# Performance work log

Measured on AMD Instinct MI355X. Metric: run time of the kernel, lower is better.

The kernel has to match this reference:

```python
import jax, jax.numpy as jnp
import numpy as np

KERNEL = 3072
STRIDE = 512


def setup_inputs() -> dict:
    key = jax.random.key(0)
    ks = jax.random.split(key, 8)
    B, Cin, L = 8, 4, 524288
    Cout, H = 512, 512
    return {
        "input": jax.random.normal(ks[0], (B, Cin, L), jnp.float32),
        "hidden": jnp.zeros((1, B, H), jnp.float32),
        "conv_w": jax.random.normal(ks[1], (Cout, Cin, KERNEL), jnp.float32) * 0.01,
        "conv_b": jax.random.normal(ks[2], (Cout,), jnp.float32) * 0.01,
        "w_ih": jax.random.normal(ks[3], (3 * H, Cout), jnp.float32) * 0.04,
        "w_hh": jax.random.normal(ks[4], (3 * H, H), jnp.float32) * 0.04,
        "b_ih": jax.random.normal(ks[5], (3 * H,), jnp.float32) * 0.04,
        "b_hh": jax.random.normal(ks[6], (3 * H,), jnp.float32) * 0.04,
    }


def _gru_scan(x_tbc, h0, w_ih, w_hh, b_ih, b_hh):
    # PyTorch GRU cell semantics, batched over B, scanned over T.
    # Precompute input projections for all timesteps: [T, B, 3H]
    gi = jnp.einsum('tbc,gc->tbg', x_tbc, w_ih) + b_ih

    def step(h, gi_t):
        gh = h @ w_hh.T + b_hh  # [B, 3H]
        i_r, i_z, i_n = jnp.split(gi_t, 3, axis=-1)
        h_r, h_z, h_n = jnp.split(gh, 3, axis=-1)
        r = jax.nn.sigmoid(i_r + h_r)
        z = jax.nn.sigmoid(i_z + h_z)
        n = jnp.tanh(i_n + r * h_n)
        h_new = (1.0 - z) * n + z * h
        return h_new, h_new

    hT, ys = jax.lax.scan(step, h0, gi)
    return ys, hT


def reference(input, hidden, conv_w, conv_b, w_ih, w_hh, b_ih, b_hh):
    # Conv1d stem: [B, Cin, L] -> [B, Cout, T]
    out = jax.lax.conv_general_dilated(
        input, conv_w, window_strides=(STRIDE,), padding='VALID',
        dimension_numbers=('NCH', 'OIH', 'NCH'))
    out = out + conv_b[None, :, None]
    # dropout is identity in eval mode
    x = jnp.moveaxis(out, 2, 0)  # [T, B, Cout]
    h0 = hidden[0]  # [B, H]
    ys, hT = _gru_scan(x, h0, w_ih, w_hh, b_ih, b_hh)  # ys: [T, B, H]
    T, B, H = ys.shape
    # torch.cat of T tensors [1, B, H] along dim=1 -> [1, T*B, H]
    return ys.reshape(1, T * B, H), hT[None]
```

## Files before the change

kernel.cpp:

```cpp
#include <hip/hip_runtime.h>
#include <hip/hip_fp16.h>
#include <hip/hip_bf16.h>

#define TSTEPS 1019
#define BATCH 8
#define CIN 4
#define LEN 524288
#define COUT 512
#define HID 512
#define KERN 3072
#define CSTRIDE 512
#define KTOT (CIN * KERN)
#define MROWS (TSTEPS * BATCH)

typedef _Float16 half2_v __attribute__((ext_vector_type(2)));
typedef __attribute__((ext_vector_type(8))) short bf16x8;
typedef __attribute__((ext_vector_type(4))) float f32x4;

#if defined(__has_builtin)
#if __has_builtin(__builtin_amdgcn_fdot2)
#define HAVE_FDOT2 1
#endif
#endif

__device__ __forceinline__ float dot2f(__half2 a, __half2 b, float c) {
#ifdef HAVE_FDOT2
    return __builtin_amdgcn_fdot2(__builtin_bit_cast(half2_v, a),
                                  __builtin_bit_cast(half2_v, b), c, false);
#else
    float2 af = __half22float2(a), bf = __half22float2(b);
    return fmaf(af.y, bf.y, fmaf(af.x, bf.x, c));
#endif
}

struct __align__(16) H2x4 { __half2 x, y, z, w; };

__device__ __forceinline__ short bfc(float x) {
    return (short)__builtin_bit_cast(unsigned short, __float2bfloat16(x));
}

__device__ __forceinline__ void load_lds16(const unsigned short* g, unsigned short* l) {
    __builtin_amdgcn_global_load_lds(
        (const __attribute__((address_space(1))) void*)g,
        (__attribute__((address_space(3))) void*)l, 16, 0, 0);
}

__global__ __launch_bounds__(256) void f2bf_k(
        const float* __restrict__ a, unsigned short* __restrict__ o, int n4) {
    int i = blockIdx.x * blockDim.x + threadIdx.x;
    int stride = gridDim.x * blockDim.x;
    for (; i < n4; i += stride) {
        float4 f = reinterpret_cast<const float4*>(a)[i];
        ushort4 u;
        u.x = (unsigned short)bfc(f.x); u.y = (unsigned short)bfc(f.y);
        u.z = (unsigned short)bfc(f.z); u.w = (unsigned short)bfc(f.w);
        reinterpret_cast<ushort4*>(o)[i] = u;
    }
}

__global__ __launch_bounds__(256, 2) void conv_mfma_k(
        const float* __restrict__ in, const unsigned short* __restrict__ wb,
        const float* __restrict__ bias, unsigned short* __restrict__ out) {
    __shared__ unsigned short At[2][128 * 64];
    __shared__ unsigned short Bt[2][128 * 64];
    const int m0 = blockIdx.y * 128;
    const int n0 = blockIdx.x * 128;
    const int tid = threadIdx.x;
    const int w = tid >> 6, l = tid & 63;
    const int wm = w >> 1, wn = w & 1;
    const int fr = l & 15, fq = l >> 4;

    const int ra = tid >> 1, hh = tid & 1;
    int mA = m0 + ra; if (mA > MROWS - 1) mA = MROWS - 1;
    const int tA = mA >> 3, bA = mA & 7;

    f32x4 acc[4][4] = {};

    const int NT = KTOT / 64;

    {
        const int k0 = 0, ci = 0, kr = 0;
        const float* src = in + (size_t)(bA * CIN + ci) * LEN
                              + (size_t)tA * CSTRIDE + kr + hh * 32;
        #pragma unroll
        for (int cc = 0; cc < 4; ++cc) {
            float4 f0 = reinterpret_cast<const float4*>(src)[cc * 2];
            float4 f1 = reinterpret_cast<const float4*>(src)[cc * 2 + 1];
            bf16x8 v;
            v[0] = bfc(f0.x); v[1] = bfc(f0.y); v[2] = bfc(f0.z); v[3] = bfc(f0.w);
            v[4] = bfc(f1.x); v[5] = bfc(f1.y); v[6] = bfc(f1.z); v[7] = bfc(f1.w);
            const int c = hh * 4 + cc, s = c ^ (ra & 7);
            *reinterpret_cast<bf16x8*>(&At[0][ra * 64 + s * 8]) = v;
        }
        #pragma unroll
        for (int i = 0; i < 4; ++i) {
            const int rb = w * 32 + i * 8 + (l >> 3);
            const int s = l & 7, c = s ^ (rb & 7);
            load_lds16(wb + (size_t)(n0 + rb) * KTOT + k0 + c * 8,
                       &Bt[0][(w * 32 + i * 8) * 64]);
        }
    }
    __syncthreads();

    int cur = 0;
    for (int t = 0; t < NT; ++t) {
        const int nxt = cur ^ 1;
        float4 fA[8];
        const bool more = (t + 1 < NT);
        if (more) {
            const int k0 = (t + 1) * 64;
            const int ci = k0 / KERN, kr = k0 - ci * KERN;
            const float* src = in + (size_t)(bA * CIN + ci) * LEN
                                  + (size_t)tA * CSTRIDE + kr + hh * 32;
            #pragma unroll
            for (int v = 0; v < 8; ++v)
                fA[v] = reinterpret_cast<const float4*>(src)[v];
            #pragma unroll
            for (int i = 0; i < 4; ++i) {
                const int rb = w * 32 + i * 8 + (l >> 3);
                const int s = l & 7, c = s ^ (rb & 7);
                load_lds16(wb + (size_t)(n0 + rb) * KTOT + k0 + c * 8,
                           &Bt[nxt][(w * 32 + i * 8) * 64]);
            }
        }
        #pragma unroll
        for (int ks = 0; ks < 2; ++ks) {
            bf16x8 af[4], bfg[4];
            #pragma unroll
            for (int mf = 0; mf < 4; ++mf) {
                const int rA = wm * 64 + mf * 16 + fr;
                const int cw = ks * 4 + fq, s = cw ^ (rA & 7);
                af[mf] = *reinterpret_cast<const bf16x8*>(&At[cur][rA * 64 + s * 8]);
            }
            #pragma unroll
            for (int nf = 0; nf < 4; ++nf) {
                const int rB = wn * 64 + nf * 16 + fr;
                const int cw = ks * 4 + fq, s = cw ^ (rB & 7);
                bfg[nf] = *reinterpret_cast<const bf16x8*>(&Bt[cur][rB * 64 + s * 8]);
            }
            #pragma unroll
            for (int mf = 0; mf < 4; ++mf)
                #pragma unroll
                for (int nf = 0; nf < 4; ++nf)
                    acc[mf][nf] = __builtin_amdgcn_mfma_f32_16x16x32_bf16(
                        af[mf], bfg[nf], acc[mf][nf], 0, 0, 0);
        }
        if (more) {
            #pragma unroll
            for (int cc = 0; cc < 4; ++cc) {
                float4 f0 = fA[cc * 2], f1 = fA[cc * 2 + 1];
                bf16x8 v;
                v[0] = bfc(f0.x); v[1] = bfc(f0.y); v[2] = bfc(f0.z); v[3] = bfc(f0.w);
                v[4] = bfc(f1.x); v[5] = bfc(f1.y); v[6] = bfc(f1.z); v[7] = bfc(f1.w);
                const int c = hh * 4 + cc, s = c ^ (ra & 7);
                *reinterpret_cast<bf16x8*>(&At[nxt][ra * 64 + s * 8]) = v;
            }
        }
        __syncthreads();
        cur = nxt;
    }

    #pragma unroll
    for (int nf = 0; nf < 4; ++nf) {
        const int n = n0 + wn * 64 + nf * 16 + fr;
        const float bv = bias[n];
        #pragma unroll
        for (int mf = 0; mf < 4; ++mf) {
            #pragma unroll
            for (int i = 0; i < 4; ++i) {
                const int m = m0 + wm * 64 + mf * 16 + fq * 4 + i;
                if (m < MROWS)
                    out[(size_t)m * COUT + n] =
                        (unsigned short)bfc(acc[mf][nf][i] + bv);
            }
        }
    }
}

__global__ __launch_bounds__(256, 2) void proj_mfma_k(
        const unsigned short* __restrict__ A, const unsigned short* __restrict__ wb,
        const float* __restrict__ bias, float* __restrict__ out) {
    __shared__ unsigned short At[2][128 * 64];
    __shared__ unsigned short Bt[2][128 * 64];
    const int m0 = blockIdx.y * 128;
    const int n0 = blockIdx.x * 128;
    const int tid = threadIdx.x;
    const int w = tid >> 6, l = tid & 63;
    const int wm = w >> 1, wn = w & 1;
    const int fr = l & 15, fq = l >> 4;

    f32x4 acc[4][4] = {};
    const int NT = COUT / 64;

    auto stage = [&](int buf, int k0) {
        #pragma unroll
        for (int i = 0; i < 4; ++i) {
            const int r = w * 32 + i * 8 + (l >> 3);
            const int s = l & 7, c = s ^ (r & 7);
            int mA = m0 + r; if (mA > MROWS - 1) mA = MROWS - 1;
            load_lds16(A + (size_t)mA * COUT + k0 + c * 8,
                       &At[buf][(w * 32 + i * 8) * 64]);
            load_lds16(wb + (size_t)(n0 + r) * COUT + k0 + c * 8,
                       &Bt[buf][(w * 32 + i * 8) * 64]);
        }
    };

    stage(0, 0);
    __syncthreads();
    int cur = 0;
    for (int t = 0; t < NT; ++t) {
        const int nxt = cur ^ 1;
        if (t + 1 < NT) stage(nxt, (t + 1) * 64);
        #pragma unroll
        for (int ks = 0; ks < 2; ++ks) {
            bf16x8 af[4], bfg[4];
            #pragma unroll
            for (int mf = 0; mf < 4; ++mf) {
                const int rA = wm * 64 + mf * 16 + fr;
                const int cw = ks * 4 + fq, s = cw ^ (rA & 7);
                af[mf] = *reinterpret_cast<const bf16x8*>(&At[cur][rA * 64 + s * 8]);
            }
            #pragma unroll
            for (int nf = 0; nf < 4; ++nf) {
                const int rB = wn * 64 + nf * 16 + fr;
                const int cw = ks * 4 + fq, s = cw ^ (rB & 7);
                bfg[nf] = *reinterpret_cast<const bf16x8*>(&Bt[cur][rB * 64 + s * 8]);
            }
            #pragma unroll
            for (int mf = 0; mf < 4; ++mf)
                #pragma unroll
                for (int nf = 0; nf < 4; ++nf)
                    acc[mf][nf] = __builtin_amdgcn_mfma_f32_16x16x32_bf16(
                        af[mf], bfg[nf], acc[mf][nf], 0, 0, 0);
        }
        __syncthreads();
        cur = nxt;
    }

    #pragma unroll
    for (int nf = 0; nf < 4; ++nf) {
        const int n = n0 + wn * 64 + nf * 16 + fr;
        const float bv = bias[n];
        #pragma unroll
        for (int mf = 0; mf < 4; ++mf) {
            #pragma unroll
            for (int i = 0; i < 4; ++i) {
                const int m = m0 + wm * 64 + mf * 16 + fq * 4 + i;
                if (m < MROWS)
                    out[(size_t)m * 1536 + n] = acc[mf][nf][i] + bv;
            }
        }
    }
}

__global__ __launch_bounds__(512, 1) void gru_scan_k(
        const float* __restrict__ gi, const float* __restrict__ w_hh,
        const float* __restrict__ b_hh, const float* __restrict__ hidden,
        float* __restrict__ out, unsigned long long* __restrict__ h_ex) {
    const int bid = blockIdx.x;
    const int b   = bid & 7;
    const int isl = bid >> 3;
    const int tid = threadIdx.x;
    const int q   = tid >> 7;
    const int g   = tid & 127;
    const int j   = isl * 128 + g;

    __shared__ __align__(16) __half2 hh2[256];
    __shared__ float p_lds[1920];

    __half2 wreg[3][64];
    #pragma unroll
    for (int m = 0; m < 3; ++m) {
        const float* wp = w_hh + (size_t)(j + m * 512) * HID + q * 128;
        #pragma unroll
        for (int kk = 0; kk < 32; ++kk) {
            float4 v = reinterpret_cast<const float4*>(wp)[kk];
            wreg[m][2 * kk]     = __halves2half2(__float2half_rn(v.x), __float2half_rn(v.y));
            wreg[m][2 * kk + 1] = __halves2half2(__float2half_rn(v.z), __float2half_rn(v.w));
        }
    }

    float bhr = 0.f, bhz = 0.f, bhn = 0.f, hprev = 0.f;
    if (tid < 128) {
        bhr = b_hh[j]; bhz = b_hh[j + 512]; bhn = b_hh[j + 1024];
        hprev = hidden[b * HID + j];
    }
    if (tid < 256) {
        float h0a = hidden[b * HID + 2 * tid];
        float h0b = hidden[b * HID + 2 * tid + 1];
        hh2[tid] = __halves2half2(__float2half(h0a), __float2half(h0b));
    }
    __syncthreads();

    float gir = 0.f, giz = 0.f, gin = 0.f;
    if (tid < 128) {
        const float* gp = gi + (size_t)b * 1536 + j;
        gir = gp[0]; giz = gp[512]; gin = gp[1024];
    }

    for (int t = 0; t < TSTEPS; ++t) {
        const H2x4* hv4 = reinterpret_cast<const H2x4*>(hh2 + q * 64);
        float a0 = 0, a1 = 0, a2 = 0, c0 = 0, c1 = 0, c2 = 0;
        #pragma unroll
        for (int kk = 0; kk < 16; ++kk) {
            H2x4 h4 = hv4[kk];
            a0 = dot2f(wreg[0][4 * kk + 0], h4.x, a0);
            a1 = dot2f(wreg[1][4 * kk + 0], h4.x, a1);
            a2 = dot2f(wreg[2][4 * kk + 0], h4.x, a2);
            c0 = dot2f(wreg[0][4 * kk + 1], h4.y, c0);
            c1 = dot2f(wreg[1][4 * kk + 1], h4.y, c1);
            c2 = dot2f(wreg[2][4 * kk + 1], h4.y, c2);
            a0 = dot2f(wreg[0][4 * kk + 2], h4.z, a0);
            a1 = dot2f(wreg[1][4 * kk + 2], h4.z, a1);
            a2 = dot2f(wreg[2][4 * kk + 2], h4.z, a2);
            c0 = dot2f(wreg[0][4 * kk + 3], h4.w, c0);
            c1 = dot2f(wreg[1][4 * kk + 3], h4.w, c1);
            c2 = dot2f(wreg[2][4 * kk + 3], h4.w, c2);
        }
        p_lds[(0 * 128 + g) * 5 + q] = a0 + c0;
        p_lds[(1 * 128 + g) * 5 + q] = a1 + c1;
        p_lds[(2 * 128 + g) * 5 + q] = a2 + c2;
        __syncthreads();

        float hnew = 0.f;
        if (tid < 128) {
            const float* pr = &p_lds[(0 * 128 + tid) * 5];
            const float* pz = &p_lds[(1 * 128 + tid) * 5];
            const float* pn = &p_lds[(2 * 128 + tid) * 5];
            const float ghr = pr[0] + pr[1] + pr[2] + pr[3] + bhr;
            const float ghz = pz[0] + pz[1] + pz[2] + pz[3] + bhz;
            const float ghn = pn[0] + pn[1] + pn[2] + pn[3] + bhn;
            const float r = 1.f / (1.f + __expf(-(gir + ghr)));
            const float z = 1.f / (1.f + __expf(-(giz + ghz)));
            const float nx = gin + r * ghn;
            const float n = 1.f - 2.f / (__expf(2.f * nx) + 1.f);
            hnew = (1.f - z) * n + z * hprev;
            hprev = hnew;
            out[(size_t)(t * BATCH + b) * HID + j] = hnew;
            float hother = __shfl_xor(hnew, 1);
            if (!(tid & 1) && t < TSTEPS - 1) {
                unsigned long long* pub = h_ex
                    + (size_t)(((t + 1) & 1) * BATCH + b) * 256
                    + isl * 64 + (tid >> 1);
                __half2 h2 = __halves2half2(__float2half(hnew), __float2half(hother));
                unsigned long long v =
                    ((unsigned long long)(unsigned)(t + 1) << 32) |
                    (unsigned long long)__builtin_bit_cast(unsigned, h2);
                __hip_atomic_store(pub, v, __ATOMIC_RELAXED,
                                   __HIP_MEMORY_SCOPE_AGENT);
            }
        }
        if (t == TSTEPS - 1) break;

        if (tid < 128) {
            const float* gp = gi + (size_t)((t + 1) * BATCH + b) * 1536 + j;
            gir = gp[0]; giz = gp[512]; gin = gp[1024];
        }

        if (tid < 256) {
            unsigned long long* src = h_ex
                + (size_t)(((t + 1) & 1) * BATCH + b) * 256 + tid;
            unsigned long long v;
            do {
                v = __hip_atomic_load(src, __ATOMIC_RELAXED,
                                      __HIP_MEMORY_SCOPE_AGENT);
            } while ((unsigned)(v >> 32) != (unsigned)(t + 1));
            hh2[tid] = __builtin_bit_cast(__half2, (unsigned)(v & 0xffffffffu));
        }
        __syncthreads();
    }
    if (tid < 128)
        out[(size_t)TSTEPS * BATCH * HID + b * HID + j] = hprev;
}

extern "C" void kernel_launch(void* const* d_in, const int* in_sizes, int n_in,
                              void* d_out, int out_size, void* d_ws, size_t ws_size,
                              hipStream_t stream) {
    (void)in_sizes; (void)n_in; (void)out_size; (void)ws_size;
    const float* input  = (const float*)d_in[0];
    const float* hidden = (const float*)d_in[1];
    const float* conv_w = (const float*)d_in[2];
    const float* conv_b = (const float*)d_in[3];
    const float* w_ih   = (const float*)d_in[4];
    const float* w_hh   = (const float*)d_in[5];
    const float* b_ih   = (const float*)d_in[6];
    const float* b_hh   = (const float*)d_in[7];
    float* out = (float*)d_out;

    char* ws = (char*)d_ws;
    float*          gi       = (float*)ws;
    unsigned short* conv_out = (unsigned short*)(ws + 50085888);
    unsigned short* w_bf     = (unsigned short*)(ws + 58433536);
    unsigned short* wih_bf   = (unsigned short*)(ws + 71016448);
    unsigned long long* h_ex = (unsigned long long*)(ws + 72589312);

    f2bf_k<<<2048, 256, 0, stream>>>(conv_w, w_bf, KTOT * COUT / 4);
    f2bf_k<<<768, 256, 0, stream>>>(w_ih, wih_bf, 1536 * COUT / 4);

    dim3 cgrid(4, 64);
    conv_mfma_k<<<cgrid, 256, 0, stream>>>(input, w_bf, conv_b, conv_out);

    dim3 pgrid(12, 64);
    proj_mfma_k<<<pgrid, 256, 0, stream>>>(conv_out, wih_bf, b_ih, gi);

    hipMemsetAsync(h_ex, 0, 32768, stream);

    gru_scan_k<<<32, 512, 0, stream>>>(gi, w_hh, b_hh, hidden, out, h_ex);
}
```

Measured before the change: 2.208 ms.

## Interleave two batch rows per GRU block to overlap polling with compute

The GRU scan is re-partitioned so that each block handles two batch rows and a 64-wide hidden slice instead of one row and a 128-wide slice. Rows are grouped into teams of 8 blocks. Each block alternates between its two rows within a timestep, so waiting for the other blocks' hidden state for one row overlaps with the matvec and gates of the other row. The per-thread register weight slice is halved, and the partial-sum reduction grows from 4 to 8 terms. In exchange there are more barriers per step, and the block count and launch config may need to match the unseen host code.

Result: slower. 3.178 ms (+43.9%).

```diff
diff --git a/kernel.cpp b/kernel.cpp
--- a/kernel.cpp
+++ b/kernel.cpp
@@ -75,13 +75,11 @@
     const int tA = mA >> 3, bA = mA & 7;
 
     f32x4 acc[4][4] = {};
-
     const int NT = KTOT / 64;
 
     {
-        const int k0 = 0, ci = 0, kr = 0;
-        const float* src = in + (size_t)(bA * CIN + ci) * LEN
-                              + (size_t)tA * CSTRIDE + kr + hh * 32;
+        const float* src = in + (size_t)(bA * CIN + 0) * LEN
+                              + (size_t)tA * CSTRIDE + 0 + hh * 32;
         #pragma unroll
         for (int cc = 0; cc < 4; ++cc) {
             float4 f0 = reinterpret_cast<const float4*>(src)[cc * 2];
@@ -96,7 +94,7 @@
         for (int i = 0; i < 4; ++i) {
             const int rb = w * 32 + i * 8 + (l >> 3);
             const int s = l & 7, c = s ^ (rb & 7);
-            load_lds16(wb + (size_t)(n0 + rb) * KTOT + k0 + c * 8,
+            load_lds16(wb + (size_t)(n0 + rb) * KTOT + 0 + c * 8,
                        &Bt[0][(w * 32 + i * 8) * 64]);
         }
     }
@@ -253,124 +251,145 @@
     }
 }
 
+#define MATVEC(PB)                                                            \
+    do {                                                                      \
+        const H2x4* hv4 = reinterpret_cast<const H2x4*>(&hh2[PB][q * 32]);    \
+        float a0 = 0, a1 = 0, a2 = 0, c0 = 0, c1 = 0, c2 = 0;                 \
+        _Pragma("unroll")                                                     \
+        for (int kk = 0; kk < 8; ++kk) {                                      \
+            H2x4 h4 = hv4[kk];                                                \
+            a0 = dot2f(wreg[0][4 * kk + 0], h4.x, a0);                        \
+            a1 = dot2f(wreg[1][4 * kk + 0], h4.x, a1);                        \
+            a2 = dot2f(wreg[2][4 * kk + 0], h4.x, a2);                        \
+            c0 = dot2f(wreg[0][4 * kk + 1], h4.y, c0);                        \
+            c1 = dot2f(wreg[1][4 * kk + 1], h4.y, c1);                        \
+            c2 = dot2f(wreg[2][4 * kk + 1], h4.y, c2);                        \
+            a0 = dot2f(wreg[0][4 * kk + 2], h4.z, a0);                        \
+            a1 = dot2f(wreg[1][4 * kk + 2], h4.z, a1);                        \
+            a2 = dot2f(wreg[2][4 * kk + 2], h4.z, a2);                        \
+            c0 = dot2f(wreg[0][4 * kk + 3], h4.w, c0);                        \
+            c1 = dot2f(wreg[1][4 * kk + 3], h4.w, c1);                        \
+            c2 = dot2f(wreg[2][4 * kk + 3], h4.w, c2);                        \
+        }                                                                     \
+        p_lds[(0 * 64 + g) * 9 + q] = a0 + c0;                                \
+        p_lds[(1 * 64 + g) * 9 + q] = a1 + c1;                                \
+        p_lds[(2 * 64 + g) * 9 + q] = a2 + c2;                                \
+    } while (0)
+
+#define GATE_PHASE(PB, BB)                                                    \
+    do {                                                                      \
+        const float* pr = &p_lds[(0 * 64 + tid) * 9];                         \
+        const float* pz = &p_lds[(1 * 64 + tid) * 9];                         \
+        const float* pn = &p_lds[(2 * 64 + tid) * 9];                         \
+        const float ghr = ((pr[0] + pr[1]) + (pr[2] + pr[3]))                 \
+                        + ((pr[4] + pr[5]) + (pr[6] + pr[7])) + bhr;          \
+        const float ghz = ((pz[0] + pz[1]) + (pz[2] + pz[3]))                 \
+                        + ((pz[4] + pz[5]) + (pz[6] + pz[7])) + bhz;          \
+        const float ghn = ((pn[0] + pn[1]) + (pn[2] + pn[3]))                 \
+                        + ((pn[4] + pn[5]) + (pn[6] + pn[7])) + bhn;          \
+        const float r = 1.f / (1.f + __expf(-(gir##PB + ghr)));               \
+        const float z = 1.f / (1.f + __expf(-(giz##PB + ghz)));               \
+        const float nx = gin##PB + r * ghn;                                   \
+        const float n = 1.f - 2.f / (__expf(2.f * nx) + 1.f);                 \
+        const float hnew = (1.f - z) * n + z * hprev##PB;                     \
+        hprev##PB = hnew;                                                     \
+        const float hother = __shfl_xor(hnew, 1);                             \
+        if (!(tid & 1)) {                                                     \
+            __half2 h2 = __halves2half2(__float2half(hnew),                   \
+                                        __float2half(hother));                \
+            unsigned long long v =                                            \
+                ((unsigned long long)(unsigned)(t + 1) << 32) |               \
+                (unsigned long long)__builtin_bit_cast(unsigned, h2);         \
+            __hip_atomic_store(                                               \
+                h_ex + (size_t)(((t + 1) & 1) * BATCH + BB) * 256             \
+                     + isl * 32 + (tid >> 1),                                 \
+                v, __ATOMIC_RELAXED, __HIP_MEMORY_SCOPE_AGENT);               \
+        }                                                                     \
+        out[(size_t)(t * BATCH + BB) * HID + j] = hnew;                       \
+        const int tn = (t + 1 < TSTEPS) ? t + 1 : t;                          \
+        const float* gp = gi + (size_t)(tn * BATCH + BB) * 1536 + j;          \
+        gir##PB = gp[0]; giz##PB = gp[512]; gin##PB = gp[1024];               \
+    } while (0)
+
+#define POLL_PHASE(PB, BB, EP)                                                \
+    do {                                                                      \
+        unsigned long long* src = h_ex                                        \
+            + (size_t)(((EP) & 1) * BATCH + BB) * 256 + tid;                  \
+        unsigned long long v;                                                 \
+        do {                                                                  \
+            v = __hip_atomic_load(src, __ATOMIC_RELAXED,                      \
+                                  __HIP_MEMORY_SCOPE_AGENT);                  \
+        } while ((unsigned)(v >> 32) != (unsigned)(EP));                      \
+        hh2[PB][tid] = __builtin_bit_cast(__half2, (unsigned)(v & 0xffffffffu)); \
+    } while (0)
+
 __global__ __launch_bounds__(512, 1) void gru_scan_k(
         const float* __restrict__ gi, const float* __restrict__ w_hh,
         const float* __restrict__ b_hh, const float* __restrict__ hidden,
         float* __restrict__ out, unsigned long long* __restrict__ h_ex) {
-    const int bid = blockIdx.x;
-    const int b   = bid & 7;
-    const int isl = bid >> 3;
+    const int bid  = blockIdx.x;
+    const int team = bid >> 3;
+    const int isl  = bid & 7;
+    const int b0 = team * 2, b1 = team * 2 + 1;
     const int tid = threadIdx.x;
-    const int q   = tid >> 7;
-    const int g   = tid & 127;
-    const int j   = isl * 128 + g;
-
-    __shared__ __align__(16) __half2 hh2[256];
-    __shared__ float p_lds[1920];
-
-    __half2 wreg[3][64];
+    const int q = tid >> 6;
+    const int g = tid & 63;
+    const int j = isl * 64 + g;
+
+    __shared__ __align__(16) __half2 hh2[2][256];
+    __shared__ float p_lds[3 * 64 * 9];
+
+    __half2 wreg[3][32];
     #pragma unroll
     for (int m = 0; m < 3; ++m) {
-        const float* wp = w_hh + (size_t)(j + m * 512) * HID + q * 128;
-        #pragma unroll
-        for (int kk = 0; kk < 32; ++kk) {
+        const float* wp = w_hh + (size_t)(j + m * 512) * HID + q * 64;
+        #pragma unroll
+        for (int kk = 0; kk < 16; ++kk) {
             float4 v = reinterpret_cast<const float4*>(wp)[kk];
             wreg[m][2 * kk]     = __halves2half2(__float2half_rn(v.x), __float2half_rn(v.y));
             wreg[m][2 * kk + 1] = __halves2half2(__float2half_rn(v.z), __float2half_rn(v.w));
         }
     }
 
-    float bhr = 0.f, bhz = 0.f, bhn = 0.f, hprev = 0.f;
-    if (tid < 128) {
+    float bhr = 0.f, bhz = 0.f, bhn = 0.f;
+    float hprev0 = 0.f, hprev1 = 0.f;
+    float gir0 = 0.f, giz0 = 0.f, gin0 = 0.f;
+    float gir1 = 0.f, giz1 = 0.f, gin1 = 0.f;
+    if (tid < 64) {
         bhr = b_hh[j]; bhz = b_hh[j + 512]; bhn = b_hh[j + 1024];
-        hprev = hidden[b * HID + j];
+        hprev0 = hidden[b0 * HID + j];
+        hprev1 = hidden[b1 * HID + j];
+        gir0 = gi[(size_t)b0 * 1536 + j];
+        giz0 = gi[(size_t)b0 * 1536 + j + 512];
+        gin0 = gi[(size_t)b0 * 1536 + j + 1024];
+        gir1 = gi[(size_t)b1 * 1536 + j];
+        giz1 = gi[(size_t)b1 * 1536 + j + 512];
+        gin1 = gi[(size_t)b1 * 1536 + j + 1024];
     }
     if (tid < 256) {
-        float h0a = hidden[b * HID + 2 * tid];
-        float h0b = hidden[b * HID + 2 * tid + 1];
-        hh2[tid] = __halves2half2(__float2half(h0a), __float2half(h0b));
+        hh2[0][tid] = __halves2half2(__float2half(hidden[b0 * HID + 2 * tid]),
+                                     __float2half(hidden[b0 * HID + 2 * tid + 1]));
+        hh2[1][tid] = __halves2half2(__float2half(hidden[b1 * HID + 2 * tid]),
+                                     __float2half(hidden[b1 * HID + 2 * tid + 1]));
     }
     __syncthreads();
 
-    float gir = 0.f, giz = 0.f, gin = 0.f;
-    if (tid < 128) {
-        const float* gp = gi + (size_t)b * 1536 + j;
-        gir = gp[0]; giz = gp[512]; gin = gp[1024];
-    }
-
     for (int t = 0; t < TSTEPS; ++t) {
-        const H2x4* hv4 = reinterpret_cast<const H2x4*>(hh2 + q * 64);
-        float a0 = 0, a1 = 0, a2 = 0, c0 = 0, c1 = 0, c2 = 0;
-        #pragma unroll
-        for (int kk = 0; kk < 16; ++kk) {
-            H2x4 h4 = hv4[kk];
-            a0 = dot2f(wreg[0][4 * kk + 0], h4.x, a0);
-            a1 = dot2f(wreg[1][4 * kk + 0], h4.x, a1);
-            a2 = dot2f(wreg[2][4 * kk + 0], h4.x, a2);
-            c0 = dot2f(wreg[0][4 * kk + 1], h4.y, c0);
-            c1 = dot2f(wreg[1][4 * kk + 1], h4.y, c1);
-            c2 = dot2f(wreg[2][4 * kk + 1], h4.y, c2);
-            a0 = dot2f(wreg[0][4 * kk + 2], h4.z, a0);
-            a1 = dot2f(wreg[1][4 * kk + 2], h4.z, a1);
-            a2 = dot2f(wreg[2][4 * kk + 2], h4.z, a2);
-            c0 = dot2f(wreg[0][4 * kk + 3], h4.w, c0);
-            c1 = dot2f(wreg[1][4 * kk + 3], h4.w, c1);
-            c2 = dot2f(wreg[2][4 * kk + 3], h4.w, c2);
-        }
-        p_lds[(0 * 128 + g) * 5 + q] = a0 + c0;
-        p_lds[(1 * 128 + g) * 5 + q] = a1 + c1;
-        p_lds[(2 * 128 + g) * 5 + q] = a2 + c2;
-        __syncthreads();
-
-        float hnew = 0.f;
-        if (tid < 128) {
-            const float* pr = &p_lds[(0 * 128 + tid) * 5];
-            const float* pz = &p_lds[(1 * 128 + tid) * 5];
-            const float* pn = &p_lds[(2 * 128 + tid) * 5];
-            const float ghr = pr[0] + pr[1] + pr[2] + pr[3] + bhr;
-            const float ghz = pz[0] + pz[1] + pz[2] + pz[3] + bhz;
-            const float ghn = pn[0] + pn[1] + pn[2] + pn[3] + bhn;
-            const float r = 1.f / (1.f + __expf(-(gir + ghr)));
-            const float z = 1.f / (1.f + __expf(-(giz + ghz)));
-            const float nx = gin + r * ghn;
-            const float n = 1.f - 2.f / (__expf(2.f * nx) + 1.f);
-            hnew = (1.f - z) * n + z * hprev;
-            hprev = hnew;
-            out[(size_t)(t * BATCH + b) * HID + j] = hnew;
-            float hother = __shfl_xor(hnew, 1);
-            if (!(tid & 1) && t < TSTEPS - 1) {
-                unsigned long long* pub = h_ex
-                    + (size_t)(((t + 1) & 1) * BATCH + b) * 256
-                    + isl * 64 + (tid >> 1);
-                __half2 h2 = __halves2half2(__float2half(hnew), __float2half(hother));
-                unsigned long long v =
-                    ((unsigned long long)(unsigned)(t + 1) << 32) |
-                    (unsigned long long)__builtin_bit_cast(unsigned, h2);
-                __hip_atomic_store(pub, v, __ATOMIC_RELAXED,
-                                   __HIP_MEMORY_SCOPE_AGENT);
-            }
-        }
-        if (t == TSTEPS - 1) break;
-
-        if (tid < 128) {
-            const float* gp = gi + (size_t)((t + 1) * BATCH + b) * 1536 + j;
-            gir = gp[0]; giz = gp[512]; gin = gp[1024];
-        }
-
-        if (tid < 256) {
-            unsigned long long* src = h_ex
-                + (size_t)(((t + 1) & 1) * BATCH + b) * 256 + tid;
-            unsigned long long v;
-            do {
-                v = __hip_atomic_load(src, __ATOMIC_RELAXED,
-                                      __HIP_MEMORY_SCOPE_AGENT);
-            } while ((unsigned)(v >> 32) != (unsigned)(t + 1));
-            hh2[tid] = __builtin_bit_cast(__half2, (unsigned)(v & 0xffffffffu));
-        }
-        __syncthreads();
-    }
-    if (tid < 128)
-        out[(size_t)TSTEPS * BATCH * HID + b * HID + j] = hprev;
+        MATVEC(0);
+        __syncthreads();
+        if (tid < 64) GATE_PHASE(0, b0);
+        if (t > 0 && tid < 256) POLL_PHASE(1, b1, t);
+        __syncthreads();
+        MATVEC(1);
+        __syncthreads();
+        if (tid < 64) GATE_PHASE(1, b1);
+        if (t + 1 < TSTEPS && tid < 256) POLL_PHASE(0, b0, t + 1);
+        __syncthreads();
+    }
+    if (tid < 64) {
+        out[(size_t)TSTEPS * BATCH * HID + b0 * HID + j] = hprev0;
+        out[(size_t)TSTEPS * BATCH * HID + b1 * HID + j] = hprev1;
+    }
 }
 
 extern "C" void kernel_launch(void* const* d_in, const int* in_sizes, int n_in,
```

## Restructure GRU scan exchange with wave-shuffle reduction and fast-path polling

Applied to the files above, without the earlier changes.

The GRU recurrent kernel now maps k-quarters to lanes within a wave, so the partial dot products are reduced with cross-lane shuffles. This removes the LDS partial-sum buffer and one block barrier per step. The hidden-state exchange double-buffers LDS, writes local halves directly, and polls remote halves with a non-coherent sc0 load before falling back to an agent-scope atomic. The next-step gi values are prefetched at the top of each step. The fast-poll path relies on cache behaviour to see updates from other blocks, and it doubles the exchange buffer.

Measured after the change: 2.872 ms. 30.1% more time.

```diff
diff --git a/kernel.cpp b/kernel.cpp
--- a/kernel.cpp
+++ b/kernel.cpp
@@ -43,6 +43,15 @@
     __builtin_amdgcn_global_load_lds(
         (const __attribute__((address_space(1))) void*)g,
         (__attribute__((address_space(3))) void*)l, 16, 0, 0);
+}
+
+__device__ __forceinline__ unsigned long long load_fast(
+        const unsigned long long* p) {
+    unsigned long long v;
+    asm volatile("global_load_dwordx2 %0, %1, off sc0\n\t"
+                 "s_waitcnt vmcnt(0)"
+                 : "=v"(v) : "v"(p) : "memory");
+    return v;
 }
 
 __global__ __launch_bounds__(256) void f2bf_k(
@@ -75,13 +84,11 @@
     const int tA = mA >> 3, bA = mA & 7;
 
     f32x4 acc[4][4] = {};
-
     const int NT = KTOT / 64;
 
     {
-        const int k0 = 0, ci = 0, kr = 0;
-        const float* src = in + (size_t)(bA * CIN + ci) * LEN
-                              + (size_t)tA * CSTRIDE + kr + hh * 32;
+        const float* src = in + (size_t)(bA * CIN + 0) * LEN
+                              + (size_t)tA * CSTRIDE + 0 + hh * 32;
         #pragma unroll
         for (int cc = 0; cc < 4; ++cc) {
             float4 f0 = reinterpret_cast<const float4*>(src)[cc * 2];
@@ -96,7 +103,7 @@
         for (int i = 0; i < 4; ++i) {
             const int rb = w * 32 + i * 8 + (l >> 3);
             const int s = l & 7, c = s ^ (rb & 7);
-            load_lds16(wb + (size_t)(n0 + rb) * KTOT + k0 + c * 8,
+            load_lds16(wb + (size_t)(n0 + rb) * KTOT + 0 + c * 8,
                        &Bt[0][(w * 32 + i * 8) * 64]);
         }
     }
@@ -261,17 +268,21 @@
     const int b   = bid & 7;
     const int isl = bid >> 3;
     const int tid = threadIdx.x;
-    const int q   = tid >> 7;
-    const int g   = tid & 127;
-    const int j   = isl * 128 + g;
-
-    __shared__ __align__(16) __half2 hh2[256];
-    __shared__ float p_lds[1920];
+    const int wv  = tid >> 6;
+    const int l   = tid & 63;
+    const int r   = l & 15;
+    const int kq  = l >> 4;
+    const int j   = isl * 128 + wv * 16 + r;
+
+    __shared__ __align__(16) __half2 hh2[2][256];
+
+    unsigned long long* hfast = h_ex;
+    unsigned long long* hslow = h_ex + 4096;
 
     __half2 wreg[3][64];
     #pragma unroll
     for (int m = 0; m < 3; ++m) {
-        const float* wp = w_hh + (size_t)(j + m * 512) * HID + q * 128;
+        const float* wp = w_hh + (size_t)(j + m * 512) * HID + kq * 128;
         #pragma unroll
         for (int kk = 0; kk < 32; ++kk) {
             float4 v = reinterpret_cast<const float4*>(wp)[kk];
@@ -280,26 +291,25 @@
         }
     }
 
-    float bhr = 0.f, bhz = 0.f, bhn = 0.f, hprev = 0.f;
-    if (tid < 128) {
-        bhr = b_hh[j]; bhz = b_hh[j + 512]; bhn = b_hh[j + 1024];
-        hprev = hidden[b * HID + j];
-    }
-    if (tid < 256) {
-        float h0a = hidden[b * HID + 2 * tid];
-        float h0b = hidden[b * HID + 2 * tid + 1];
-        hh2[tid] = __halves2half2(__float2half(h0a), __float2half(h0b));
-    }
+    const float bhr = b_hh[j], bhz = b_hh[j + 512], bhn = b_hh[j + 1024];
+    float hprev = hidden[b * HID + j];
+    float gir = gi[(size_t)b * 1536 + j];
+    float giz = gi[(size_t)b * 1536 + j + 512];
+    float gin = gi[(size_t)b * 1536 + j + 1024];
+
+    if (tid < 256)
+        hh2[0][tid] = __halves2half2(__float2half(hidden[b * HID + 2 * tid]),
+                                     __float2half(hidden[b * HID + 2 * tid + 1]));
     __syncthreads();
 
-    float gir = 0.f, giz = 0.f, gin = 0.f;
-    if (tid < 128) {
-        const float* gp = gi + (size_t)b * 1536 + j;
-        gir = gp[0]; giz = gp[512]; gin = gp[1024];
-    }
-
     for (int t = 0; t < TSTEPS; ++t) {
-        const H2x4* hv4 = reinterpret_cast<const H2x4*>(hh2 + q * 64);
+        const bool more = (t + 1 < TSTEPS);
+        float ngr = 0.f, ngz = 0.f, ngn = 0.f;
+        if (more) {
+            const float* gp = gi + (size_t)((t + 1) * BATCH + b) * 1536 + j;
+            ngr = gp[0]; ngz = gp[512]; ngn = gp[1024];
+        }
+        const H2x4* hv4 = reinterpret_cast<const H2x4*>(&hh2[t & 1][0]) + kq * 16;
         float a0 = 0, a1 = 0, a2 = 0, c0 = 0, c1 = 0, c2 = 0;
         #pragma unroll
         for (int kk = 0; kk < 16; ++kk) {
@@ -317,59 +327,60 @@
             c1 = dot2f(wreg[1][4 * kk + 3], h4.w, c1);
             c2 = dot2f(wreg[2][4 * kk + 3], h4.w, c2);
         }
-        p_lds[(0 * 128 + g) * 5 + q] = a0 + c0;
-        p_lds[(1 * 128 + g) * 5 + q] = a1 + c1;
-        p_lds[(2 * 128 + g) * 5 + q] = a2 + c2;
+        float ghr = a0 + c0, ghz = a1 + c1, ghn = a2 + c2;
+        ghr += __shfl_xor(ghr, 16); ghr += __shfl_xor(ghr, 32);
+        ghz += __shfl_xor(ghz, 16); ghz += __shfl_xor(ghz, 32);
+        ghn += __shfl_xor(ghn, 16); ghn += __shfl_xor(ghn, 32);
+        const float rr = 1.f / (1.f + __expf(-(gir + ghr + bhr)));
+        const float zz = 1.f / (1.f + __expf(-(giz + ghz + bhz)));
+        const float nx = gin + rr * (ghn + bhn);
+        const float nn = 1.f - 2.f / (__expf(2.f * nx) + 1.f);
+        const float hnew = (1.f - zz) * nn + zz * hprev;
+        hprev = hnew;
+        gir = ngr; giz = ngz; gin = ngn;
+        const float hother = __shfl_xor(hnew, 1);
+
+        if (kq == 0) {
+            out[(size_t)(t * BATCH + b) * HID + j] = hnew;
+            if (more && !(r & 1)) {
+                const __half2 h2 = __halves2half2(__float2half(hnew),
+                                                  __float2half(hother));
+                const unsigned pay = __builtin_bit_cast(unsigned, h2);
+                const unsigned long long v =
+                    ((unsigned long long)(unsigned)(t + 1) << 32) |
+                    (unsigned long long)pay;
+                const size_t idx =
+                    (size_t)(((t + 1) & 1) * BATCH + b) * 256 + (j >> 1);
+                hfast[idx] = v;
+                __hip_atomic_store(&hslow[idx], v, __ATOMIC_RELAXED,
+                                   __HIP_MEMORY_SCOPE_AGENT);
+                hh2[(t + 1) & 1][j >> 1] = h2;
+            }
+        }
+        if (!more) break;
+
+        if (tid < 192) {
+            const int word = tid + ((tid >= isl * 64) ? 64 : 0);
+            const size_t idx =
+                (size_t)(((t + 1) & 1) * BATCH + b) * 256 + word;
+            const int spins = (t < 2) ? 1024 : 8;
+            unsigned long long v; bool got = false;
+            for (int it = 0; it < spins; ++it) {
+                v = load_fast(&hfast[idx]);
+                if ((unsigned)(v >> 32) == (unsigned)(t + 1)) { got = true; break; }
+            }
+            if (!got) {
+                do {
+                    v = __hip_atomic_load(&hslow[idx], __ATOMIC_RELAXED,
+                                          __HIP_MEMORY_SCOPE_AGENT);
+                } while ((unsigned)(v >> 32) != (unsigned)(t + 1));
+            }
+            hh2[(t + 1) & 1][word] =
+                __builtin_bit_cast(__half2, (unsigned)(v & 0xffffffffu));
+        }
         __syncthreads();
-
-        float hnew = 0.f;
-        if (tid < 128) {
-            const float* pr = &p_lds[(0 * 128 + tid) * 5];
-            const float* pz = &p_lds[(1 * 128 + tid) * 5];
-            const float* pn = &p_lds[(2 * 128 + tid) * 5];
-            const float ghr = pr[0] + pr[1] + pr[2] + pr[3] + bhr;
-            const float ghz = pz[0] + pz[1] + pz[2] + pz[3] + bhz;
-            const float ghn = pn[0] + pn[1] + pn[2] + pn[3] + bhn;
-            const float r = 1.f / (1.f + __expf(-(gir + ghr)));
-            const float z = 1.f / (1.f + __expf(-(giz + ghz)));
-            const float nx = gin + r * ghn;
-            const float n = 1.f - 2.f / (__expf(2.f * nx) + 1.f);
-            hnew = (1.f - z) * n + z * hprev;
-            hprev = hnew;
-            out[(size_t)(t * BATCH + b) * HID + j] = hnew;
-            float hother = __shfl_xor(hnew, 1);
-            if (!(tid & 1) && t < TSTEPS - 1) {
-                unsigned long long* pub = h_ex
-                    + (size_t)(((t + 1) & 1) * BATCH + b) * 256
-                    + isl * 64 + (tid >> 1);
-                __half2 h2 = __halves2half2(__float2half(hnew), __float2half(hother));
-                unsigned long long v =
-                    ((unsigned long long)(unsigned)(t + 1) << 32) |
-                    (unsigned long long)__builtin_bit_cast(unsigned, h2);
-                __hip_atomic_store(pub, v, __ATOMIC_RELAXED,
-                                   __HIP_MEMORY_SCOPE_AGENT);
-            }
-        }
-        if (t == TSTEPS - 1) break;
-
-        if (tid < 128) {
-            const float* gp = gi + (size_t)((t + 1) * BATCH + b) * 1536 + j;
-            gir = gp[0]; giz = gp[512]; gin = gp[1024];
-        }
-
-        if (tid < 256) {
-            unsigned long long* src = h_ex
-                + (size_t)(((t + 1) & 1) * BATCH + b) * 256 + tid;
-            unsigned long long v;
-            do {
-                v = __hip_atomic_load(src, __ATOMIC_RELAXED,
-                                      __HIP_MEMORY_SCOPE_AGENT);
-            } while ((unsigned)(v >> 32) != (unsigned)(t + 1));
-            hh2[tid] = __builtin_bit_cast(__half2, (unsigned)(v & 0xffffffffu));
-        }
-        __syncthreads();
-    }
-    if (tid < 128)
+    }
+    if (kq == 0)
         out[(size_t)TSTEPS * BATCH * HID + b * HID + j] = hprev;
 }
 
@@ -403,7 +414,7 @@
     dim3 pgrid(12, 64);
     proj_mfma_k<<<pgrid, 256, 0, stream>>>(conv_out, wih_bf, b_ih, gi);
 
-    hipMemsetAsync(h_ex, 0, 32768, stream);
+    hipMemsetAsync(h_ex, 0, 65536, stream);
 
     gru_scan_k<<<32, 512, 0, stream>>>(gi, w_hh, b_hh, hidden, out, h_ex);
 }
```

## Widen GRU scan blocks to 1024 threads with shuffle reduction and double-buffered hidden state

Applied to the files above, without the earlier changes.

The recurrent GRU kernel now runs 1024 threads per block, so each thread holds half as many w_hh weights and does half the dot-product work per step. Partial sums are reduced across lanes with shuffles before a smaller LDS reduction. The hidden-state buffer is double-buffered, and each block writes its own slice locally instead of re-reading it from global memory. Fewer threads spin on the cross-block exchange, the aim being a shorter per-timestep critical path, at the cost of more threads per block and an extra shuffle stage.

Result: slower. 2.844 ms (+28.8%).

```diff
diff --git a/kernel.cpp b/kernel.cpp
--- a/kernel.cpp
+++ b/kernel.cpp
@@ -75,13 +75,11 @@
     const int tA = mA >> 3, bA = mA & 7;
 
     f32x4 acc[4][4] = {};
-
     const int NT = KTOT / 64;
 
     {
-        const int k0 = 0, ci = 0, kr = 0;
-        const float* src = in + (size_t)(bA * CIN + ci) * LEN
-                              + (size_t)tA * CSTRIDE + kr + hh * 32;
+        const float* src = in + (size_t)(bA * CIN + 0) * LEN
+                              + (size_t)tA * CSTRIDE + 0 + hh * 32;
         #pragma unroll
         for (int cc = 0; cc < 4; ++cc) {
             float4 f0 = reinterpret_cast<const float4*>(src)[cc * 2];
@@ -96,7 +94,7 @@
         for (int i = 0; i < 4; ++i) {
             const int rb = w * 32 + i * 8 + (l >> 3);
             const int s = l & 7, c = s ^ (rb & 7);
-            load_lds16(wb + (size_t)(n0 + rb) * KTOT + k0 + c * 8,
+            load_lds16(wb + (size_t)(n0 + rb) * KTOT + 0 + c * 8,
                        &Bt[0][(w * 32 + i * 8) * 64]);
         }
     }
@@ -253,7 +251,7 @@
     }
 }
 
-__global__ __launch_bounds__(512, 1) void gru_scan_k(
+__global__ __launch_bounds__(1024, 4) void gru_scan_k(
         const float* __restrict__ gi, const float* __restrict__ w_hh,
         const float* __restrict__ b_hh, const float* __restrict__ hidden,
         float* __restrict__ out, unsigned long long* __restrict__ h_ex) {
@@ -261,48 +259,54 @@
     const int b   = bid & 7;
     const int isl = bid >> 3;
     const int tid = threadIdx.x;
-    const int q   = tid >> 7;
-    const int g   = tid & 127;
-    const int j   = isl * 128 + g;
-
-    __shared__ __align__(16) __half2 hh2[256];
-    __shared__ float p_lds[1920];
-
-    __half2 wreg[3][64];
+    const int wv  = tid >> 6;
+    const int l   = tid & 63;
+    const int r   = l & 15;
+    const int ck  = l >> 4;
+    const int rg  = wv & 7;
+    const int kh  = wv >> 3;
+    const int row = rg * 16 + r;
+    const int j   = isl * 128 + row;
+    const int g8  = kh * 4 + ck;
+
+    __shared__ __align__(16) __half2 hh2[2][288];
+    __shared__ float p_lds[128 * 7];
+
+    __half2 wreg[3][32];
     #pragma unroll
     for (int m = 0; m < 3; ++m) {
-        const float* wp = w_hh + (size_t)(j + m * 512) * HID + q * 128;
-        #pragma unroll
-        for (int kk = 0; kk < 32; ++kk) {
+        const float* wp = w_hh + (size_t)(j + m * 512) * HID + kh * 256 + ck * 64;
+        #pragma unroll
+        for (int kk = 0; kk < 16; ++kk) {
             float4 v = reinterpret_cast<const float4*>(wp)[kk];
             wreg[m][2 * kk]     = __halves2half2(__float2half_rn(v.x), __float2half_rn(v.y));
             wreg[m][2 * kk + 1] = __halves2half2(__float2half_rn(v.z), __float2half_rn(v.w));
         }
     }
 
+    const int jg = isl * 128 + (tid & 127);
     float bhr = 0.f, bhz = 0.f, bhn = 0.f, hprev = 0.f;
-    if (tid < 128) {
-        bhr = b_hh[j]; bhz = b_hh[j + 512]; bhn = b_hh[j + 1024];
-        hprev = hidden[b * HID + j];
-    }
-    if (tid < 256) {
-        float h0a = hidden[b * HID + 2 * tid];
-        float h0b = hidden[b * HID + 2 * tid + 1];
-        hh2[tid] = __halves2half2(__float2half(h0a), __float2half(h0b));
-    }
-    __syncthreads();
-
     float gir = 0.f, giz = 0.f, gin = 0.f;
     if (tid < 128) {
-        const float* gp = gi + (size_t)b * 1536 + j;
-        gir = gp[0]; giz = gp[512]; gin = gp[1024];
-    }
+        bhr = b_hh[jg]; bhz = b_hh[jg + 512]; bhn = b_hh[jg + 1024];
+        hprev = hidden[b * HID + jg];
+        gir = gi[(size_t)b * 1536 + jg];
+        giz = gi[(size_t)b * 1536 + jg + 512];
+        gin = gi[(size_t)b * 1536 + jg + 1024];
+    }
+    if (tid < 256) {
+        __half2 h2 = __halves2half2(__float2half(hidden[b * HID + 2 * tid]),
+                                    __float2half(hidden[b * HID + 2 * tid + 1]));
+        hh2[0][(tid >> 5) * 36 + (tid & 31)] = h2;
+    }
+    __syncthreads();
 
     for (int t = 0; t < TSTEPS; ++t) {
-        const H2x4* hv4 = reinterpret_cast<const H2x4*>(hh2 + q * 64);
+        const bool more = (t + 1 < TSTEPS);
+        const H2x4* hv4 = reinterpret_cast<const H2x4*>(&hh2[t & 1][g8 * 36]);
         float a0 = 0, a1 = 0, a2 = 0, c0 = 0, c1 = 0, c2 = 0;
         #pragma unroll
-        for (int kk = 0; kk < 16; ++kk) {
+        for (int kk = 0; kk < 8; ++kk) {
             H2x4 h4 = hv4[kk];
             a0 = dot2f(wreg[0][4 * kk + 0], h4.x, a0);
             a1 = dot2f(wreg[1][4 * kk + 0], h4.x, a1);
@@ -317,60 +321,63 @@
             c1 = dot2f(wreg[1][4 * kk + 3], h4.w, c1);
             c2 = dot2f(wreg[2][4 * kk + 3], h4.w, c2);
         }
-        p_lds[(0 * 128 + g) * 5 + q] = a0 + c0;
-        p_lds[(1 * 128 + g) * 5 + q] = a1 + c1;
-        p_lds[(2 * 128 + g) * 5 + q] = a2 + c2;
+        float s0 = a0 + c0, s1 = a1 + c1, s2 = a2 + c2;
+        s0 += __shfl_xor(s0, 16); s0 += __shfl_xor(s0, 32);
+        s1 += __shfl_xor(s1, 16); s1 += __shfl_xor(s1, 32);
+        s2 += __shfl_xor(s2, 16); s2 += __shfl_xor(s2, 32);
+        if (l < 16) {
+            p_lds[row * 7 + 0 + kh] = s0;
+            p_lds[row * 7 + 2 + kh] = s1;
+            p_lds[row * 7 + 4 + kh] = s2;
+        }
         __syncthreads();
 
-        float hnew = 0.f;
         if (tid < 128) {
-            const float* pr = &p_lds[(0 * 128 + tid) * 5];
-            const float* pz = &p_lds[(1 * 128 + tid) * 5];
-            const float* pn = &p_lds[(2 * 128 + tid) * 5];
-            const float ghr = pr[0] + pr[1] + pr[2] + pr[3] + bhr;
-            const float ghz = pz[0] + pz[1] + pz[2] + pz[3] + bhz;
-            const float ghn = pn[0] + pn[1] + pn[2] + pn[3] + bhn;
-            const float r = 1.f / (1.f + __expf(-(gir + ghr)));
-            const float z = 1.f / (1.f + __expf(-(giz + ghz)));
-            const float nx = gin + r * ghn;
-            const float n = 1.f - 2.f / (__expf(2.f * nx) + 1.f);
-            hnew = (1.f - z) * n + z * hprev;
+            const float* pp = &p_lds[tid * 7];
+            const float ghr = pp[0] + pp[1] + bhr;
+            const float ghz = pp[2] + pp[3] + bhz;
+            const float ghn = pp[4] + pp[5] + bhn;
+            const float rr = 1.f / (1.f + __expf(-(gir + ghr)));
+            const float zz = 1.f / (1.f + __expf(-(giz + ghz)));
+            const float nx = gin + rr * ghn;
+            const float nn = 1.f - 2.f / (__expf(2.f * nx) + 1.f);
+            const float hnew = (1.f - zz) * nn + zz * hprev;
             hprev = hnew;
-            out[(size_t)(t * BATCH + b) * HID + j] = hnew;
-            float hother = __shfl_xor(hnew, 1);
-            if (!(tid & 1) && t < TSTEPS - 1) {
-                unsigned long long* pub = h_ex
-                    + (size_t)(((t + 1) & 1) * BATCH + b) * 256
-                    + isl * 64 + (tid >> 1);
-                __half2 h2 = __halves2half2(__float2half(hnew), __float2half(hother));
-                unsigned long long v =
+            const float hother = __shfl_xor(hnew, 1);
+            const __half2 h2 = __halves2half2(__float2half(hnew),
+                                              __float2half(hother));
+            if (more && !(tid & 1)) {
+                const unsigned long long v =
                     ((unsigned long long)(unsigned)(t + 1) << 32) |
                     (unsigned long long)__builtin_bit_cast(unsigned, h2);
-                __hip_atomic_store(pub, v, __ATOMIC_RELAXED,
-                                   __HIP_MEMORY_SCOPE_AGENT);
-            }
-        }
-        if (t == TSTEPS - 1) break;
-
-        if (tid < 128) {
-            const float* gp = gi + (size_t)((t + 1) * BATCH + b) * 1536 + j;
-            gir = gp[0]; giz = gp[512]; gin = gp[1024];
-        }
-
-        if (tid < 256) {
-            unsigned long long* src = h_ex
-                + (size_t)(((t + 1) & 1) * BATCH + b) * 256 + tid;
+                const int w0 = isl * 64 + (tid >> 1);
+                __hip_atomic_store(
+                    h_ex + (size_t)(((t + 1) & 1) * BATCH + b) * 256 + w0,
+                    v, __ATOMIC_RELAXED, __HIP_MEMORY_SCOPE_AGENT);
+                hh2[(t + 1) & 1][(w0 >> 5) * 36 + (w0 & 31)] = h2;
+            }
+            out[(size_t)(t * BATCH + b) * HID + jg] = hnew;
+            if (more) {
+                const float* gp = gi + (size_t)((t + 1) * BATCH + b) * 1536 + jg;
+                gir = gp[0]; giz = gp[512]; gin = gp[1024];
+            }
+        } else if (tid < 320 && more) {
+            const int i = tid - 128;
+            const int w0 = i + ((i >= isl * 64) ? 64 : 0);
+            const unsigned long long* src =
+                h_ex + (size_t)(((t + 1) & 1) * BATCH + b) * 256 + w0;
             unsigned long long v;
             do {
                 v = __hip_atomic_load(src, __ATOMIC_RELAXED,
                                       __HIP_MEMORY_SCOPE_AGENT);
             } while ((unsigned)(v >> 32) != (unsigned)(t + 1));
-            hh2[tid] = __builtin_bit_cast(__half2, (unsigned)(v & 0xffffffffu));
+            hh2[(t + 1) & 1][(w0 >> 5) * 36 + (w0 & 31)] =
+                __builtin_bit_cast(__half2, (unsigned)(v & 0xffffffffu));
         }
         __syncthreads();
     }
     if (tid < 128)
-        out[(size_t)TSTEPS * BATCH * HID + b * HID + j] = hprev;
+        out[(size_t)TSTEPS * BATCH * HID + b * HID + jg] = hprev;
 }
 
 extern "C" void kernel_launch(void* const* d_in, const int* in_sizes, int n_in,
@@ -405,5 +412,5 @@
 
     hipMemsetAsync(h_ex, 0, 32768, stream);
 
-    gru_scan_k<<<32, 512, 0, stream>>>(gi, w_hh, b_hh, hidden, out, h_ex);
-}
+    gru_scan_k<<<32, 1024, 0, stream>>>(gi, w_hh, b_hh, hidden, out, h_ex);
+}
```
